# Optimization experiments

Measured on AMD Instinct MI355X. Metric: run time of the kernel, lower is better.

## Reference

```python
import jax, jax.numpy as jnp
import numpy as np

B, S, H, K = 16, 1024, 1024, 256


def _span(x, Ws, bs, start, end):
    # x: [B,S,H]; start/end: [B,K] int indices into the S axis
    def proj(W, b):
        return jnp.einsum('bsh,oh->bso', x, W) + b  # nn.Linear: x @ W.T + b

    def gather(p, idx):
        # batched index_select along seq axis -> [B,K,H]
        return jnp.take_along_axis(p, idx[..., None], axis=1)

    p1, p2, p3, p4 = (proj(W, b) for W, b in zip(Ws, bs))
    span = (gather(p1, start) + gather(p2, end)
            + (gather(p3, start) - gather(p3, end))
            + gather(p4, start) * gather(p4, end))
    return jnp.tanh(span)


def setup_inputs() -> dict:
    key = jax.random.key(0)
    ks = jax.random.split(key, 20)
    inp = {
        'hidden_states': jax.random.normal(ks[0], (B, S, H), dtype=jnp.float32),
        'prem_word_idxs': jax.random.randint(ks[1], (B, 1, 2, K), 0, S, dtype=jnp.int64) if jax.config.read('jax_enable_x64') else jax.random.randint(ks[1], (B, 1, 2, K), 0, S).astype(jnp.int32),
        'hypo_word_idxs': jax.random.randint(ks[2], (B, 1, 2, K), 0, S).astype(jnp.int32),
    }
    names = ['Wp1', 'bp1', 'Wp2', 'bp2', 'Wp3', 'bp3', 'Wp4', 'bp4',
             'Wh1', 'bh1', 'Wh2', 'bh2', 'Wh3', 'bh3', 'Wh4', 'bh4']
    for i, n in enumerate(names):
        k = ks[3 + i]
        if n.startswith('W'):
            inp[n] = jax.random.normal(k, (H, H), dtype=jnp.float32) * 0.02
        else:
            inp[n] = jax.random.normal(k, (H,), dtype=jnp.float32) * 0.02
    return inp


def reference(hidden_states, prem_word_idxs, hypo_word_idxs,
              Wp1, bp1, Wp2, bp2, Wp3, bp3, Wp4, bp4,
              Wh1, bh1, Wh2, bh2, Wh3, bh3, Wh4, bh4):
    p_idx = prem_word_idxs[:, 0]  # squeeze(1) -> [B,2,K]
    h_idx = hypo_word_idxs[:, 0]
    prem_h_ij = _span(hidden_states, (Wp1, Wp2, Wp3, Wp4), (bp1, bp2, bp3, bp4),
                      p_idx[:, 0], p_idx[:, 1])
    hypo_h_ij = _span(hidden_states, (Wh1, Wh2, Wh3, Wh4), (bh1, bh2, bh3, bh4),
                      h_idx[:, 0], h_idx[:, 1])
    return (prem_h_ij, hypo_h_ij)
```

## Files before the change

### kernel.cpp

```cpp
#include <hip/hip_runtime.h>
#include <hip/hip_bf16.h>

typedef _Float16 f16;
typedef _Float16 f16x4 __attribute__((ext_vector_type(4)));
typedef _Float16 f16x8 __attribute__((ext_vector_type(8)));
typedef float    f32x4 __attribute__((ext_vector_type(4)));

#define H_DIM 1024
#define S_DIM 1024
#define PLANE (1024*1024)
#define MT 128
#define NT 64
#define KT 32
#define AP (MT*KT)
#define ABUF (2*AP)
#define XOFF (6*PLANE)

__device__ __forceinline__ void load_lds16(const f16* g, f16* l) {
    __builtin_amdgcn_global_load_lds(
        (const __attribute__((address_space(1))) void*)g,
        (__attribute__((address_space(3))) void*)l, 16, 0, 0);
}

__global__ __launch_bounds__(256) void prep_all(
    const float* __restrict__ x,
    const float* __restrict__ Wp1, const float* __restrict__ Wp2,
    const float* __restrict__ Wp3, const float* __restrict__ Wp4,
    const float* __restrict__ Wh1, const float* __restrict__ Wh2,
    const float* __restrict__ Wh3, const float* __restrict__ Wh4,
    f16* __restrict__ ws)
{
    const int t  = threadIdx.x;
    const int bx = blockIdx.x;
    if (bx < 2048) {
        const size_t b0 = (size_t)bx * 2048;
#pragma unroll
        for (int it = 0; it < 8; ++it) {
            const size_t i = (b0 + it * 256 + t) * 4;
            f32x4 v = *(const f32x4*)(x + i);
            f16x4 h;
#pragma unroll
            for (int j = 0; j < 4; ++j) h[j] = (f16)v[j];
            *(f16x4*)(ws + XOFF + i) = h;
        }
        return;
    }
    const int wb = bx - 2048;
#pragma unroll
    for (int it = 0; it < 4; ++it) {
        const int c    = wb * 1024 + it * 256 + t;
        const int span = c >> 18;
        const size_t i = (size_t)(c & 262143) * 4;
        const float* W1 = span ? Wh1 : Wp1;
        const float* W2 = span ? Wh2 : Wp2;
        const float* W3 = span ? Wh3 : Wp3;
        const float* W4 = span ? Wh4 : Wp4;
        f16* base = ws + (size_t)span * 3 * PLANE;

        f32x4 w1 = *(const f32x4*)(W1 + i);
        f32x4 w2 = *(const f32x4*)(W2 + i);
        f32x4 w3 = *(const f32x4*)(W3 + i);
        f32x4 w4 = *(const f32x4*)(W4 + i);

        f16x4 wa, wb2, wc;
#pragma unroll
        for (int j = 0; j < 4; ++j) {
            wa[j]  = (f16)(w1[j] + w3[j]);
            wb2[j] = (f16)(w2[j] - w3[j]);
            wc[j]  = (f16)w4[j];
        }
        *(f16x4*)(base + 0*PLANE + i) = wa;
        *(f16x4*)(base + 1*PLANE + i) = wb2;
        *(f16x4*)(base + 2*PLANE + i) = wc;
    }
}

#define K_STEP(FB, FA, WCNT, FIN)                                              \
  {                                                                            \
    f16x8 afr0[4], afr1[4], bfrg[6];                                           \
    const f16* Ab = &A_all[rbA];                                               \
    _Pragma("unroll")                                                          \
    for (int mf = 0; mf < 4; ++mf) {                                           \
      int r = (wm + mf * 16 + lrow) * KT + lqs * 8;                            \
      afr0[mf] = *(const f16x8*)&Ab[r];                                        \
      afr1[mf] = *(const f16x8*)&Ab[AP + r];                                   \
    }                                                                          \
    _Pragma("unroll")                                                          \
    for (int j = 0; j < 6; ++j) {                                              \
      int p = j >> 1, nf = j & 1;                                              \
      bfrg[j] = *(const f16x8*)&B_lds[p * 2048 + (wn + nf * 16 + lrow) * KT + lqs * 8]; \
    }                                                                          \
    if (!(FIN)) {                                                              \
      __asm__ volatile("s_waitcnt lgkmcnt(0)" ::: "memory");                   \
      __builtin_amdgcn_s_barrier();                                            \
      if (FB) {                                                                \
        _Pragma("unroll")                                                      \
        for (int j = 0; j < 3; ++j) { load_lds16(bq[j], &B_lds[bdst[j]]); bq[j] += KT; } \
      }                                                                        \
      if (FA) {                                                                \
        f16* dst = &A_all[wbA];                                                \
        _Pragma("unroll")                                                      \
        for (int j = 0; j < 4; ++j) { load_lds16(ap[j], dst + adst[j]); ap[j] += KT; } \
      }                                                                        \
    }                                                                          \
    _Pragma("unroll")                                                          \
    for (int mf = 0; mf < 4; ++mf)                                             \
      _Pragma("unroll")                                                        \
      for (int nf = 0; nf < 2; ++nf) {                                         \
        accL[mf][nf] = __builtin_amdgcn_mfma_f32_16x16x32_f16(afr0[mf], bfrg[0*2+nf], accL[mf][nf], 0,0,0); \
        accL[mf][nf] = __builtin_amdgcn_mfma_f32_16x16x32_f16(afr1[mf], bfrg[1*2+nf], accL[mf][nf], 0,0,0); \
        accP[mf][nf] = __builtin_amdgcn_mfma_f32_16x16x32_f16(afr0[mf], bfrg[2*2+nf], accP[mf][nf], 0,0,0); \
        accQ[mf][nf] = __builtin_amdgcn_mfma_f32_16x16x32_f16(afr1[mf], bfrg[2*2+nf], accQ[mf][nf], 0,0,0); \
      }                                                                        \
    if (!(FIN)) {                                                              \
      __asm__ volatile("s_waitcnt vmcnt(" #WCNT ")" ::: "memory");             \
      __builtin_amdgcn_s_barrier();                                            \
      rbA = (rbA == 2 * ABUF) ? 0 : rbA + ABUF;                                \
      wbA = (wbA == 2 * ABUF) ? 0 : wbA + ABUF;                                \
    }                                                                          \
  }

__global__ __launch_bounds__(256) void span_gemm(
    const f16* __restrict__ xh,
    const int* __restrict__ idxP, const int* __restrict__ idxH,
    const f16* __restrict__ wpl,
    const float* __restrict__ bp1, const float* __restrict__ bp2, const float* __restrict__ bp4,
    const float* __restrict__ bh1, const float* __restrict__ bh2, const float* __restrict__ bh4,
    float* __restrict__ out)
{
    const int t     = threadIdx.x;
    const int mtile = blockIdx.x;
    const int ntile = blockIdx.y;
    const int span  = blockIdx.z;

    const int* idx   = span ? idxH : idxP;
    const f16* wbase = wpl + (size_t)span * 3 * PLANE;
    const float* b1 = span ? bh1 : bp1;
    const float* b2 = span ? bh2 : bp2;
    const float* b4 = span ? bh4 : bp4;
    float* obase = out + (size_t)span * 4096 * H_DIM;

    __shared__ __align__(16) f16 A_all[3 * ABUF];
    __shared__ __align__(16) f16 B_lds[3 * NT * KT];

    int* rowoff = (int*)A_all;
    {
        int side = t >> 7, m = t & 127;
        int bk = mtile * MT + m;
        int b  = bk >> 8, kk = bk & 255;
        rowoff[side * 128 + m] = (b * S_DIM + idx[b * 512 + side * 256 + kk]) * H_DIM;
    }
    __syncthreads();

    const int wid  = t >> 6;
    const int lane = t & 63;
    const int wm   = (wid & 1) * 64;
    const int wn   = (wid >> 1) * 32;
    const int lrow = lane & 15;
    const int lq   = lane >> 4;
    const int lqs  = lq ^ ((lrow >> 1) & 3);

    const int schunk = (lane & 3) ^ ((lane >> 3) & 3);

    const f16* ap[4]; int adst[4];
#pragma unroll
    for (int j = 0; j < 4; ++j) {
        int o = wid * 4 + j;
        int p = o >> 3, g = o & 7;
        int r = g * 16 + (lane >> 2);
        ap[j]   = xh + rowoff[p * 128 + r] + schunk * 8;
        adst[j] = p * AP + g * 16 * KT;
    }
    __syncthreads();

    const f16* bq[3]; int bdst[3];
#pragma unroll
    for (int j = 0; j < 3; ++j) {
        int o = wid * 3 + j;
        int p = o >> 2, g = o & 3;
        int grow = ntile * NT + g * 16 + (lane >> 2);
        bq[j]   = wbase + (size_t)p * PLANE + (size_t)grow * H_DIM + schunk * 8;
        bdst[j] = p * 2048 + g * 16 * KT;
    }

    f32x4 accL[4][2], accP[4][2], accQ[4][2];
    {
        f32x4 z = {0.f, 0.f, 0.f, 0.f};
#pragma unroll
        for (int mf = 0; mf < 4; ++mf)
#pragma unroll
            for (int nf = 0; nf < 2; ++nf) { accL[mf][nf] = z; accP[mf][nf] = z; accQ[mf][nf] = z; }
    }

#pragma unroll
    for (int j = 0; j < 4; ++j) { load_lds16(ap[j], &A_all[0 * ABUF + adst[j]]); ap[j] += KT; }
#pragma unroll
    for (int j = 0; j < 3; ++j) { load_lds16(bq[j], &B_lds[bdst[j]]); bq[j] += KT; }
#pragma unroll
    for (int j = 0; j < 4; ++j) { load_lds16(ap[j], &A_all[1 * ABUF + adst[j]]); ap[j] += KT; }
    __asm__ volatile("s_waitcnt vmcnt(4)" ::: "memory");
    __builtin_amdgcn_s_barrier();

    int rbA = 0;
    int wbA = 2 * ABUF;

    for (int ks = 0; ks < 30; ++ks) {
        K_STEP(1, 1, 4, 0);
    }
    K_STEP(1, 0, 0, 0);
    K_STEP(0, 0, 0, 1);

#pragma unroll
    for (int mf = 0; mf < 4; ++mf)
#pragma unroll
        for (int nf = 0; nf < 2; ++nf) {
            int col = ntile * NT + wn + nf * 16 + lrow;
            float bb12 = b1[col] + b2[col];
            float bb4  = b4[col];
            int row0 = mtile * MT + wm + mf * 16 + lq * 4;
#pragma unroll
            for (int i = 0; i < 4; ++i) {
                float v = accL[mf][nf][i] + bb12
                        + (accP[mf][nf][i] + bb4) * (accQ[mf][nf][i] + bb4);
                obase[(size_t)(row0 + i) * H_DIM + col] = tanhf(v);
            }
        }
}

extern "C" void kernel_launch(void* const* d_in, const int* in_sizes, int n_in,
                              void* d_out, int out_size, void* d_ws, size_t ws_size,
                              hipStream_t stream) {
    (void)in_sizes; (void)n_in; (void)out_size; (void)ws_size;
    const float* x    = (const float*)d_in[0];
    const int*   idxP = (const int*)d_in[1];
    const int*   idxH = (const int*)d_in[2];
    const float* Wp1 = (const float*)d_in[3];  const float* bp1 = (const float*)d_in[4];
    const float* Wp2 = (const float*)d_in[5];  const float* bp2 = (const float*)d_in[6];
    const float* Wp3 = (const float*)d_in[7];
    const float* Wp4 = (const float*)d_in[9];  const float* bp4 = (const float*)d_in[10];
    const float* Wh1 = (const float*)d_in[11]; const float* bh1 = (const float*)d_in[12];
    const float* Wh2 = (const float*)d_in[13]; const float* bh2 = (const float*)d_in[14];
    const float* Wh3 = (const float*)d_in[15];
    const float* Wh4 = (const float*)d_in[17]; const float* bh4 = (const float*)d_in[18];
    float* out = (float*)d_out;
    f16*   ws  = (f16*)d_ws;

    prep_all<<<2560, 256, 0, stream>>>(x, Wp1, Wp2, Wp3, Wp4,
                                       Wh1, Wh2, Wh3, Wh4, ws);
    span_gemm<<<dim3(32, 16, 2), 256, 0, stream>>>(ws + XOFF, idxP, idxH, ws,
                                                   bp1, bp2, bp4, bh1, bh2, bh4, out);
}
```

Measured before the change: 247.6 us.

## Fuse prep and GEMM into one persistent kernel with a grid barrier

Merges the fp16 conversion/weight-combining prep kernel and the span GEMM into a single 512-block kernel. The two stages are separated by an atomic-counter grid barrier, and each block now computes two adjacent N tiles with a remapped tile order. The counter lives in the last word of the output buffer, which is zeroed by a memset and later overwritten by the GEMM. This removes one kernel launch and the gap between stages. In exchange it relies on all 512 blocks being co-resident (launch_bounds 256,2) and gives up the parallelism of the larger GEMM grid.

```diff
diff --git a/kernel.cpp b/kernel.cpp
--- a/kernel.cpp
+++ b/kernel.cpp
@@ -1,5 +1,4 @@
 #include <hip/hip_runtime.h>
-#include <hip/hip_bf16.h>
 
 typedef _Float16 f16;
 typedef _Float16 f16x4 __attribute__((ext_vector_type(4)));
@@ -15,64 +14,13 @@
 #define AP (MT*KT)
 #define ABUF (2*AP)
 #define XOFF (6*PLANE)
+#define NBLK 512
+#define OUT_LAST 8388607
 
 __device__ __forceinline__ void load_lds16(const f16* g, f16* l) {
     __builtin_amdgcn_global_load_lds(
         (const __attribute__((address_space(1))) void*)g,
         (__attribute__((address_space(3))) void*)l, 16, 0, 0);
-}
-
-__global__ __launch_bounds__(256) void prep_all(
-    const float* __restrict__ x,
-    const float* __restrict__ Wp1, const float* __restrict__ Wp2,
-    const float* __restrict__ Wp3, const float* __restrict__ Wp4,
-    const float* __restrict__ Wh1, const float* __restrict__ Wh2,
-    const float* __restrict__ Wh3, const float* __restrict__ Wh4,
-    f16* __restrict__ ws)
-{
-    const int t  = threadIdx.x;
-    const int bx = blockIdx.x;
-    if (bx < 2048) {
-        const size_t b0 = (size_t)bx * 2048;
-#pragma unroll
-        for (int it = 0; it < 8; ++it) {
-            const size_t i = (b0 + it * 256 + t) * 4;
-            f32x4 v = *(const f32x4*)(x + i);
-            f16x4 h;
-#pragma unroll
-            for (int j = 0; j < 4; ++j) h[j] = (f16)v[j];
-            *(f16x4*)(ws + XOFF + i) = h;
-        }
-        return;
-    }
-    const int wb = bx - 2048;
-#pragma unroll
-    for (int it = 0; it < 4; ++it) {
-        const int c    = wb * 1024 + it * 256 + t;
-        const int span = c >> 18;
-        const size_t i = (size_t)(c & 262143) * 4;
-        const float* W1 = span ? Wh1 : Wp1;
-        const float* W2 = span ? Wh2 : Wp2;
-        const float* W3 = span ? Wh3 : Wp3;
-        const float* W4 = span ? Wh4 : Wp4;
-        f16* base = ws + (size_t)span * 3 * PLANE;
-
-        f32x4 w1 = *(const f32x4*)(W1 + i);
-        f32x4 w2 = *(const f32x4*)(W2 + i);
-        f32x4 w3 = *(const f32x4*)(W3 + i);
-        f32x4 w4 = *(const f32x4*)(W4 + i);
-
-        f16x4 wa, wb2, wc;
-#pragma unroll
-        for (int j = 0; j < 4; ++j) {
-            wa[j]  = (f16)(w1[j] + w3[j]);
-            wb2[j] = (f16)(w2[j] - w3[j]);
-            wc[j]  = (f16)w4[j];
-        }
-        *(f16x4*)(base + 0*PLANE + i) = wa;
-        *(f16x4*)(base + 1*PLANE + i) = wb2;
-        *(f16x4*)(base + 2*PLANE + i) = wc;
-    }
 }
 
 #define K_STEP(FB, FA, WCNT, FIN)                                              \
@@ -87,8 +35,8 @@
     }                                                                          \
     _Pragma("unroll")                                                          \
     for (int j = 0; j < 6; ++j) {                                              \
-      int p = j >> 1, nf = j & 1;                                              \
-      bfrg[j] = *(const f16x8*)&B_lds[p * 2048 + (wn + nf * 16 + lrow) * KT + lqs * 8]; \
+      int pp = j >> 1, nf = j & 1;                                             \
+      bfrg[j] = *(const f16x8*)&B_lds[pp * 2048 + (wn + nf * 16 + lrow) * KT + lqs * 8]; \
     }                                                                          \
     if (!(FIN)) {                                                              \
       __asm__ volatile("s_waitcnt lgkmcnt(0)" ::: "memory");                   \
@@ -120,21 +68,83 @@
     }                                                                          \
   }
 
-__global__ __launch_bounds__(256) void span_gemm(
-    const f16* __restrict__ xh,
+__global__ __launch_bounds__(256, 2) void fused_all(
+    const float* __restrict__ x,
     const int* __restrict__ idxP, const int* __restrict__ idxH,
-    const f16* __restrict__ wpl,
+    const float* __restrict__ Wp1, const float* __restrict__ Wp2,
+    const float* __restrict__ Wp3, const float* __restrict__ Wp4,
+    const float* __restrict__ Wh1, const float* __restrict__ Wh2,
+    const float* __restrict__ Wh3, const float* __restrict__ Wh4,
     const float* __restrict__ bp1, const float* __restrict__ bp2, const float* __restrict__ bp4,
     const float* __restrict__ bh1, const float* __restrict__ bh2, const float* __restrict__ bh4,
+    f16* __restrict__ ws, unsigned* __restrict__ cnt,
     float* __restrict__ out)
 {
-    const int t     = threadIdx.x;
-    const int mtile = blockIdx.x;
-    const int ntile = blockIdx.y;
-    const int span  = blockIdx.z;
+    const int p = blockIdx.x;
+    const int t = threadIdx.x;
+
+    {
+        const size_t cb = (size_t)p * 8192;
+        for (int g = 0; g < 4; ++g) {
+#pragma unroll
+            for (int k = 0; k < 8; ++k) {
+                const size_t i = (cb + (size_t)(g * 8 + k) * 256 + t) * 4;
+                f32x4 v = *(const f32x4*)(x + i);
+                f16x4 h;
+#pragma unroll
+                for (int j = 0; j < 4; ++j) h[j] = (f16)v[j];
+                *(f16x4*)(ws + XOFF + i) = h;
+            }
+        }
+#pragma unroll
+        for (int it = 0; it < 4; ++it) {
+            const int c  = p * 1024 + it * 256 + t;
+            const int sp = c >> 18;
+            const size_t i = (size_t)(c & 262143) * 4;
+            const float* W1 = sp ? Wh1 : Wp1;
+            const float* W2 = sp ? Wh2 : Wp2;
+            const float* W3 = sp ? Wh3 : Wp3;
+            const float* W4 = sp ? Wh4 : Wp4;
+            f16* base = ws + (size_t)sp * 3 * PLANE;
+
+            f32x4 w1 = *(const f32x4*)(W1 + i);
+            f32x4 w2 = *(const f32x4*)(W2 + i);
+            f32x4 w3 = *(const f32x4*)(W3 + i);
+            f32x4 w4 = *(const f32x4*)(W4 + i);
+
+            f16x4 wa, wb2, wc;
+#pragma unroll
+            for (int j = 0; j < 4; ++j) {
+                wa[j]  = (f16)(w1[j] + w3[j]);
+                wb2[j] = (f16)(w2[j] - w3[j]);
+                wc[j]  = (f16)w4[j];
+            }
+            *(f16x4*)(base + 0*PLANE + i) = wa;
+            *(f16x4*)(base + 1*PLANE + i) = wb2;
+            *(f16x4*)(base + 2*PLANE + i) = wc;
+        }
+    }
+
+    __syncthreads();
+    if (t == 0) {
+        __threadfence();
+        unsigned v = atomicAdd(cnt, 1u) + 1u;
+        while (v < NBLK) {
+            __builtin_amdgcn_s_sleep(2);
+            v = atomicAdd(cnt, 0u);
+        }
+    }
+    __syncthreads();
+    __threadfence();
+
+    const int L     = ((p & 63) << 3) | (p >> 6);
+    const int nt0   = (L & 7) * 2;
+    const int mtile = (L >> 3) & 31;
+    const int span  = L >> 8;
 
     const int* idx   = span ? idxH : idxP;
-    const f16* wbase = wpl + (size_t)span * 3 * PLANE;
+    const f16* wbase = ws + (size_t)span * 3 * PLANE;
+    const f16* xh    = ws + XOFF;
     const float* b1 = span ? bh1 : bp1;
     const float* b2 = span ? bh2 : bp2;
     const float* b4 = span ? bh4 : bp4;
@@ -159,72 +169,78 @@
     const int lrow = lane & 15;
     const int lq   = lane >> 4;
     const int lqs  = lq ^ ((lrow >> 1) & 3);
-
     const int schunk = (lane & 3) ^ ((lane >> 3) & 3);
 
-    const f16* ap[4]; int adst[4];
+    const f16* apb[4]; int adst[4];
 #pragma unroll
     for (int j = 0; j < 4; ++j) {
         int o = wid * 4 + j;
-        int p = o >> 3, g = o & 7;
+        int pl = o >> 3, g = o & 7;
         int r = g * 16 + (lane >> 2);
-        ap[j]   = xh + rowoff[p * 128 + r] + schunk * 8;
-        adst[j] = p * AP + g * 16 * KT;
-    }
-    __syncthreads();
-
-    const f16* bq[3]; int bdst[3];
-#pragma unroll
-    for (int j = 0; j < 3; ++j) {
-        int o = wid * 3 + j;
-        int p = o >> 2, g = o & 3;
-        int grow = ntile * NT + g * 16 + (lane >> 2);
-        bq[j]   = wbase + (size_t)p * PLANE + (size_t)grow * H_DIM + schunk * 8;
-        bdst[j] = p * 2048 + g * 16 * KT;
-    }
-
-    f32x4 accL[4][2], accP[4][2], accQ[4][2];
-    {
-        f32x4 z = {0.f, 0.f, 0.f, 0.f};
+        apb[j]  = xh + rowoff[pl * 128 + r] + schunk * 8;
+        adst[j] = pl * AP + g * 16 * KT;
+    }
+
+    for (int ti = 0; ti < 2; ++ti) {
+        const int ntile = nt0 + ti;
+        __syncthreads();
+
+        const f16* bq[3]; int bdst[3];
+#pragma unroll
+        for (int j = 0; j < 3; ++j) {
+            int o = wid * 3 + j;
+            int pl = o >> 2, g = o & 3;
+            int grow = ntile * NT + g * 16 + (lane >> 2);
+            bq[j]   = wbase + (size_t)pl * PLANE + (size_t)grow * H_DIM + schunk * 8;
+            bdst[j] = pl * 2048 + g * 16 * KT;
+        }
+        const f16* ap[4];
+#pragma unroll
+        for (int j = 0; j < 4; ++j) ap[j] = apb[j];
+
+        f32x4 accL[4][2], accP[4][2], accQ[4][2];
+        {
+            f32x4 z = {0.f, 0.f, 0.f, 0.f};
+#pragma unroll
+            for (int mf = 0; mf < 4; ++mf)
+#pragma unroll
+                for (int nf = 0; nf < 2; ++nf) { accL[mf][nf] = z; accP[mf][nf] = z; accQ[mf][nf] = z; }
+        }
+
+#pragma unroll
+        for (int j = 0; j < 4; ++j) { load_lds16(ap[j], &A_all[0 * ABUF + adst[j]]); ap[j] += KT; }
+#pragma unroll
+        for (int j = 0; j < 3; ++j) { load_lds16(bq[j], &B_lds[bdst[j]]); bq[j] += KT; }
+#pragma unroll
+        for (int j = 0; j < 4; ++j) { load_lds16(ap[j], &A_all[1 * ABUF + adst[j]]); ap[j] += KT; }
+        __asm__ volatile("s_waitcnt vmcnt(4)" ::: "memory");
+        __builtin_amdgcn_s_barrier();
+
+        int rbA = 0;
+        int wbA = 2 * ABUF;
+
+        for (int ks = 0; ks < 30; ++ks) {
+            K_STEP(1, 1, 4, 0);
+        }
+        K_STEP(1, 0, 0, 0);
+        K_STEP(0, 0, 0, 1);
+
 #pragma unroll
         for (int mf = 0; mf < 4; ++mf)
 #pragma unroll
-            for (int nf = 0; nf < 2; ++nf) { accL[mf][nf] = z; accP[mf][nf] = z; accQ[mf][nf] = z; }
-    }
-
-#pragma unroll
-    for (int j = 0; j < 4; ++j) { load_lds16(ap[j], &A_all[0 * ABUF + adst[j]]); ap[j] += KT; }
-#pragma unroll
-    for (int j = 0; j < 3; ++j) { load_lds16(bq[j], &B_lds[bdst[j]]); bq[j] += KT; }
-#pragma unroll
-    for (int j = 0; j < 4; ++j) { load_lds16(ap[j], &A_all[1 * ABUF + adst[j]]); ap[j] += KT; }
-    __asm__ volatile("s_waitcnt vmcnt(4)" ::: "memory");
-    __builtin_amdgcn_s_barrier();
-
-    int rbA = 0;
-    int wbA = 2 * ABUF;
-
-    for (int ks = 0; ks < 30; ++ks) {
-        K_STEP(1, 1, 4, 0);
-    }
-    K_STEP(1, 0, 0, 0);
-    K_STEP(0, 0, 0, 1);
-
-#pragma unroll
-    for (int mf = 0; mf < 4; ++mf)
-#pragma unroll
-        for (int nf = 0; nf < 2; ++nf) {
-            int col = ntile * NT + wn + nf * 16 + lrow;
-            float bb12 = b1[col] + b2[col];
-            float bb4  = b4[col];
-            int row0 = mtile * MT + wm + mf * 16 + lq * 4;
-#pragma unroll
-            for (int i = 0; i < 4; ++i) {
-                float v = accL[mf][nf][i] + bb12
-                        + (accP[mf][nf][i] + bb4) * (accQ[mf][nf][i] + bb4);
-                obase[(size_t)(row0 + i) * H_DIM + col] = tanhf(v);
+            for (int nf = 0; nf < 2; ++nf) {
+                int col = ntile * NT + wn + nf * 16 + lrow;
+                float bb12 = b1[col] + b2[col];
+                float bb4  = b4[col];
+                int row0 = mtile * MT + wm + mf * 16 + lq * 4;
+#pragma unroll
+                for (int i = 0; i < 4; ++i) {
+                    float v = accL[mf][nf][i] + bb12
+                            + (accP[mf][nf][i] + bb4) * (accQ[mf][nf][i] + bb4);
+                    obase[(size_t)(row0 + i) * H_DIM + col] = tanhf(v);
+                }
             }
-        }
+    }
 }
 
 extern "C" void kernel_launch(void* const* d_in, const int* in_sizes, int n_in,
@@ -244,9 +260,12 @@
     const float* Wh4 = (const float*)d_in[17]; const float* bh4 = (const float*)d_in[18];
     float* out = (float*)d_out;
     f16*   ws  = (f16*)d_ws;
-
-    prep_all<<<2560, 256, 0, stream>>>(x, Wp1, Wp2, Wp3, Wp4,
-                                       Wh1, Wh2, Wh3, Wh4, ws);
-    span_gemm<<<dim3(32, 16, 2), 256, 0, stream>>>(ws + XOFF, idxP, idxH, ws,
-                                                   bp1, bp2, bp4, bh1, bh2, bh4, out);
+    unsigned* cnt = (unsigned*)out + OUT_LAST;
+
+    hipMemsetAsync((void*)cnt, 0, 4, stream);
+    fused_all<<<NBLK, 256, 0, stream>>>(x, idxP, idxH,
+                                        Wp1, Wp2, Wp3, Wp4,
+                                        Wh1, Wh2, Wh3, Wh4,
+                                        bp1, bp2, bp4, bh1, bh2, bh4,
+                                        ws, cnt, out);
 }
```

After: 324.2 us. +30.9%, slower.
